# Performance work log

Hardware: AMD Instinct MI355X
Metric: run time of the kernel (lower is better)

The kernel has to match this reference:

```python
import jax, jax.numpy as jnp
import numpy as np

# Paged/ragged causal prefill attention (FlashInfer wrapper.run semantics),
# modeled as equal-length batched causal GQA attention.
B, S = 2, 2048          # batch, seq_len (T = B*S tokens, flattened)
H, HKV, D = 32, 8, 128  # query heads, kv heads, head dim
G = H // HKV            # GQA group size
SCALE = 0.08838834764831845  # 1/sqrt(D)


def setup_inputs() -> dict:
    key = jax.random.key(0)
    kq, kk, kv = jax.random.split(key, 3)
    q = jax.random.normal(kq, (B * S, H * D), dtype=jnp.float32)
    k = jax.random.normal(kk, (B * S, HKV * D), dtype=jnp.float32)
    v = jax.random.normal(kv, (B * S, HKV * D), dtype=jnp.float32)
    return {"q": q, "k": k, "v": v}


def reference(q, k, v):
    # q: [T, H*D] -> [B, S, HKV, G, D]; k, v: [T, HKV*D] -> [B, S, HKV, D]
    qh = q.reshape(B, S, HKV, G, D)
    kh = k.reshape(B, S, HKV, D)
    vh = v.reshape(B, S, HKV, D)
    # GQA attention scores: [B, HKV, G, Sq, Sk]
    scores = jnp.einsum('bqhgd,bkhd->bhgqk', qh, kh) * SCALE
    causal = jnp.tril(jnp.ones((S, S), dtype=bool))  # query attends to keys <= its position
    scores = jnp.where(causal, scores, jnp.finfo(scores.dtype).min)
    probs = jax.nn.softmax(scores, axis=-1)
    out = jnp.einsum('bhgqk,bkhd->bqhgd', probs, vh)
    # back to flattened token layout [T, H*D]
    return out.reshape(B * S, H * D)
```

## Files before the change

### kernel.cpp

```cpp
#include <hip/hip_runtime.h>


#define B_   2
#define S_   2048
#define H_   32
#define HKV_ 8
#define D_   128
#define SCALEF 0.08838834764831845f
#define COEF  (SCALEF * 1.44269504088896340736f)
#define DEFER_THR 8.0f

typedef float          f32x4 __attribute__((ext_vector_type(4)));
typedef __bf16         bf16x4 __attribute__((ext_vector_type(4)));
typedef __bf16         bf16x8 __attribute__((ext_vector_type(8)));
typedef unsigned short u16x8 __attribute__((ext_vector_type(8)));

#define MFMA16(a, b, c) __builtin_amdgcn_mfma_f32_16x16x32_bf16((a), (b), (c), 0, 0, 0)

#if defined(__has_builtin)
#if __has_builtin(__builtin_amdgcn_exp2f)
#define EXP2F(x) __builtin_amdgcn_exp2f(x)
#endif
#endif
#ifndef EXP2F
#define EXP2F(x) exp2f(x)
#endif

static __device__ __forceinline__ unsigned short f2bf(float f) {
  unsigned int u = __builtin_bit_cast(unsigned int, f);
  u = (u + 0x7fffu + ((u >> 16) & 1u)) >> 16;
  return (unsigned short)u;
}

static __device__ __forceinline__ void load_lds16(const void* g, void* l) {
  __builtin_amdgcn_global_load_lds(
      (const __attribute__((address_space(1))) void*)g,
      (__attribute__((address_space(3))) void*)l, 16, 0, 0);
}

static __device__ __forceinline__ float swz_x16(float v) {
  return __builtin_bit_cast(
      float, __builtin_amdgcn_ds_swizzle(__builtin_bit_cast(int, v), 0x401F));
}
static __device__ __forceinline__ float bperm_f(int byteaddr, float v) {
  return __builtin_bit_cast(
      float,
      __builtin_amdgcn_ds_bpermute(byteaddr, __builtin_bit_cast(int, v)));
}

__global__ __launch_bounds__(256) void prep_kernel(
    const float* __restrict__ k, const float* __restrict__ v,
    unsigned short* __restrict__ kbf, unsigned short* __restrict__ vt) {
  __shared__ float tile[32][65];
  const int tid = threadIdx.x;
  const int gid = (int)blockIdx.x;
  if (gid < 2048) {
    int t = gid * 256 + tid;
    int o = t * 8;
    int d = o & (D_ - 1);
    int s = (o >> 7) & (S_ - 1);
    int bh = o >> 18;
    int b = bh >> 3, hkv = bh & 7;
    const float* src = k + (size_t)(b * S_ + s) * (HKV_ * D_) + hkv * D_ + d;
    f32x4 x0 = *(const f32x4*)src;
    f32x4 x1 = *(const f32x4*)(src + 4);
    u16x8 w;
    w[0] = f2bf(x0[0]); w[1] = f2bf(x0[1]); w[2] = f2bf(x0[2]); w[3] = f2bf(x0[3]);
    w[4] = f2bf(x1[0]); w[5] = f2bf(x1[1]); w[6] = f2bf(x1[2]); w[7] = f2bf(x1[3]);
    *(u16x8*)(kbf + o) = w;
  } else {
    const int t = gid - 2048;
    const int s0 = (t & 31) * 64;
    const int d0 = ((t >> 5) & 3) * 32;
    const int bh = t >> 7;
    const float* src = v + (size_t)(bh >> 3) * S_ * (HKV_ * D_) + (bh & 7) * D_;
#pragma unroll
    for (int it = 0; it < 8; ++it) {
      int idx = it * 256 + tid;
      int sl = idx >> 5, dl = idx & 31;
      tile[dl][sl] = src[(size_t)(s0 + sl) * (HKV_ * D_) + d0 + dl];
    }
    __syncthreads();
    unsigned int* dst = (unsigned int*)vt;
#pragma unroll
    for (int it = 0; it < 4; ++it) {
      int idx = it * 256 + tid;
      int dl = idx >> 5, sp = idx & 31;
      unsigned int w = (unsigned int)f2bf(tile[dl][2 * sp]) |
                       ((unsigned int)f2bf(tile[dl][2 * sp + 1]) << 16);
      dst[(((size_t)bh * D_ + d0 + dl) * S_ + s0 + 2 * sp) >> 1] = w;
    }
  }
}

__global__ __launch_bounds__(256, 4) void attn_kernel(
    const float* __restrict__ qg, const unsigned short* __restrict__ kbfg,
    const unsigned short* __restrict__ vtg, float* __restrict__ outg) {
  __shared__ unsigned short KL[2][32 * 128];
  __shared__ unsigned short VL[2][128 * 32];

  const int tid = threadIdx.x;
  const int wave = tid >> 6, lane = tid & 63;
  const int l15 = lane & 15, quad = lane >> 4;
  const int a32 = ((lane ^ 32) << 2);
  const int rowa = quad << 4;

  const int id = (int)blockIdx.x + 16 * (int)blockIdx.y;
  const int xcd = id & 7, slot = id >> 3;
  const int bhkv = xcd * 2 + (slot >> 6);
  const int inner = slot & 63;
  const int g = inner >> 4;
  const int xb = inner & 15;
  const int b = bhkv >> 3, hkv = bhkv & 7;
  const int h = hkv * 4 + g;

  const unsigned short* kbf = kbfg + (size_t)(b * HKV_ + hkv) * S_ * D_;
  const unsigned short* vtb = vtg + (size_t)(b * HKV_ + hkv) * D_ * S_;

  const f32x4 zero4 = {0.f, 0.f, 0.f, 0.f};
  const float NEG_INF = -__builtin_huge_valf();

  auto stage = [&](int kt, int buf) {
#pragma unroll
    for (int j = 0; j < 2; ++j) {
      int si = wave * 128 + j * 64 + lane;
      int kr = si >> 4, pc = si & 15;
      int lc = pc ^ (kr & 15);
      int gs = ((kr & 15) >> 2) * 8 + ((kr >> 4) << 2) + (kr & 3);
      load_lds16(kbf + (size_t)(kt * 32 + gs) * D_ + lc * 8,
                 &KL[buf][(wave * 128 + j * 64) * 8]);
    }
#pragma unroll
    for (int j = 0; j < 2; ++j) {
      int si = wave * 128 + j * 64 + lane;
      int dr = si >> 2, pc = si & 3;
      int lc = pc ^ ((dr >> 1) & 3);
      load_lds16(vtb + (size_t)dr * S_ + kt * 32 + lc * 8,
                 &VL[buf][(wave * 128 + j * 64) * 8]);
    }
  };

  for (int ph = 0; ph < 2; ++ph) {
    const int qb = ph ? (31 - xb) : xb;
    const int qbase = qb * 64 + wave * 16;
    const int qgp = qbase + l15;

    bf16x8 qf[4];
#pragma unroll
    for (int ch = 0; ch < 4; ++ch) {
      const float* p = qg + (size_t)(b * S_ + qbase + l15) * (H_ * D_) +
                       h * D_ + ch * 32 + quad * 8;
      f32x4 x0 = *(const f32x4*)p;
      f32x4 x1 = *(const f32x4*)(p + 4);
      bf16x8 t;
      t[0] = (__bf16)(x0[0] * COEF); t[1] = (__bf16)(x0[1] * COEF);
      t[2] = (__bf16)(x0[2] * COEF); t[3] = (__bf16)(x0[3] * COEF);
      t[4] = (__bf16)(x1[0] * COEF); t[5] = (__bf16)(x1[1] * COEF);
      t[6] = (__bf16)(x1[2] * COEF); t[7] = (__bf16)(x1[3] * COEF);
      qf[ch] = t;
    }

    f32x4 acc[8];
#pragma unroll
    for (int dt = 0; dt < 8; ++dt) acc[dt] = zero4;
    float mrow = NEG_INF;
    float lsum = 0.f;

    const int nkt = qb * 2 + 2;

    stage(0, 0);
    __syncthreads();

#define KITER(KT, CUR)                                                        \
  do {                                                                        \
    const int kt_ = (KT);                                                     \
    if (kt_ + 1 < nkt) stage(kt_ + 1, (CUR) ^ 1);                             \
    if (kt_ * 32 <= qbase + 15) {                                             \
      f32x4 sc[2] = {zero4, zero4};                                           \
      __builtin_amdgcn_s_setprio(1);                                          \
      _Pragma("unroll") for (int h2 = 0; h2 < 2; ++h2) {                      \
        const int row = h2 * 16 + l15;                                        \
        _Pragma("unroll") for (int ch = 0; ch < 4; ++ch) {                    \
          const int pc = (ch * 4 + quad) ^ l15;               \
          u16x8 kf = *(const u16x8*)&KL[(CUR)][row * D_ + pc * 8];            \
          sc[h2] = MFMA16(__builtin_bit_cast(bf16x8, kf), qf[ch], sc[h2]);    \
        }                                                                     \
      }                                                                       \
      __builtin_amdgcn_s_setprio(0);                                          \
      const int kb0 = kt_ * 32;                                               \
                       \
      _Pragma("unroll") for (int h2 = 0; h2 < 2; ++h2) {                      \
        if (kb0 + 27 + h2 * 4 > qbase) {                                      \
          int kb2 = kb0 + quad * 8 + h2 * 4;                                  \
          _Pragma("unroll") for (int r = 0; r < 4; ++r) {                     \
            if (kb2 + r > qgp) sc[h2][r] = NEG_INF;                           \
          }                                                                   \
        }                                                                     \
      }                                                                       \
                      \
      float l8 = fmaxf(fmaxf(fmaxf(sc[0][0], sc[0][1]),                       \
                             fmaxf(sc[0][2], sc[0][3])),                      \
                       fmaxf(fmaxf(sc[1][0], sc[1][1]),                       \
                             fmaxf(sc[1][2], sc[1][3])));                     \
      if (!__all(l8 <= mrow + DEFER_THR)) {                                   \
        float t = fmaxf(l8, swz_x16(l8));             \
        t = fmaxf(t, bperm_f(a32, t));                                        \
        float mn = fmaxf(mrow, t);                                            \
        float al = EXP2F(mrow - mn);                                          \
        mrow = mn;                                                            \
        lsum *= al;                                                           \
        f32x4 av;       \
        _Pragma("unroll") for (int r = 0; r < 4; ++r)                         \
            av[r] = bperm_f(rowa + (r << 2), al);                             \
        _Pragma("unroll") for (int dt = 0; dt < 8; ++dt)                      \
            _Pragma("unroll") for (int r = 0; r < 4; ++r)                     \
                acc[dt][r] *= av[r];                                          \
      }                                                                       \
                         \
      _Pragma("unroll") for (int h2 = 0; h2 < 2; ++h2)                        \
          _Pragma("unroll") for (int r = 0; r < 4; ++r)                       \
              sc[h2][r] = EXP2F(sc[h2][r] - mrow);                            \
      lsum += ((sc[0][0] + sc[0][1]) + (sc[0][2] + sc[0][3])) +               \
              ((sc[1][0] + sc[1][1]) + (sc[1][2] + sc[1][3]));                \
             \
      bf16x8 pb;                                                              \
      pb[0] = (__bf16)sc[0][0]; pb[1] = (__bf16)sc[0][1];                     \
      pb[2] = (__bf16)sc[0][2]; pb[3] = (__bf16)sc[0][3];                     \
      pb[4] = (__bf16)sc[1][0]; pb[5] = (__bf16)sc[1][1];                     \
      pb[6] = (__bf16)sc[1][2]; pb[7] = (__bf16)sc[1][3];                     \
                       \
      {                                                                       \
        const int vsw = (quad ^ ((l15 >> 1) & 3)) * 8;                        \
        __builtin_amdgcn_s_setprio(1);                                        \
        _Pragma("unroll") for (int dt = 0; dt < 8; ++dt) {                    \
          u16x8 vf = *(const u16x8*)&VL[(CUR)][(dt * 16 + l15) * 32 + vsw];   \
          acc[dt] = MFMA16(pb, __builtin_bit_cast(bf16x8, vf), acc[dt]);      \
        }                                                                     \
        __builtin_amdgcn_s_setprio(0);                                        \
      }                                                                       \
    }                                                                         \
    __syncthreads();  \
  } while (0)

    for (int kt = 0; kt < nkt; kt += 2) {
      KITER(kt, 0);
      KITER(kt + 1, 1);
    }
#undef KITER

    float s = lsum;
    s += swz_x16(s);
    s += bperm_f(a32, s);
    float linv = 1.0f / s;
    f32x4 inv;
#pragma unroll
    for (int r = 0; r < 4; ++r) inv[r] = bperm_f(rowa + (r << 2), linv);
#pragma unroll
    for (int dt = 0; dt < 8; ++dt)
#pragma unroll
      for (int r = 0; r < 4; ++r)
        outg[(size_t)(b * S_ + qbase + quad * 4 + r) * (H_ * D_) +
             h * D_ + dt * 16 + l15] = acc[dt][r] * inv[r];
  }
}

extern "C" void kernel_launch(void* const* d_in, const int* in_sizes, int n_in,
                              void* d_out, int out_size, void* d_ws,
                              size_t ws_size, hipStream_t stream) {
  const float* q = (const float*)d_in[0];
  const float* k = (const float*)d_in[1];
  const float* v = (const float*)d_in[2];
  float* out = (float*)d_out;
  unsigned short* kws = (unsigned short*)d_ws;
  unsigned short* vtws = kws + (size_t)B_ * HKV_ * S_ * D_;

  prep_kernel<<<4096, 256, 0, stream>>>(k, v, kws, vtws);

  dim3 g2(16, B_ * H_);
  attn_kernel<<<g2, 256, 0, stream>>>(q, kws, vtws, out);
}
```

Baseline: 221.2 us.

## Software-pipeline QK^T of next tile with softmax and PV of previous tile

Restructures the KV loop so each iteration computes QK^T scores for the current tile while running softmax and PV on the previous tile's scores, which overlaps MFMA work with exp/reduction work. V moves to a triple-buffered LDS ring so the previous tile's V stays resident while the next one is being staged. This costs extra LDS and registers for the second score set, which may lower occupancy, and adds a tail step after the loop plus a barrier at the start of each phase.

After: 227.7 us. 1.03x slower.

```diff
diff --git a/kernel.cpp b/kernel.cpp
--- a/kernel.cpp
+++ b/kernel.cpp
@@ -97,7 +97,7 @@
     const float* __restrict__ qg, const unsigned short* __restrict__ kbfg,
     const unsigned short* __restrict__ vtg, float* __restrict__ outg) {
   __shared__ unsigned short KL[2][32 * 128];
-  __shared__ unsigned short VL[2][128 * 32];
+  __shared__ unsigned short VL[3][128 * 32];
 
   const int tid = threadIdx.x;
   const int wave = tid >> 6, lane = tid & 63;
@@ -120,7 +120,7 @@
   const f32x4 zero4 = {0.f, 0.f, 0.f, 0.f};
   const float NEG_INF = -__builtin_huge_valf();
 
-  auto stage = [&](int kt, int buf) {
+  auto stage = [&](int kt, int kbuf, int vbuf) {
 #pragma unroll
     for (int j = 0; j < 2; ++j) {
       int si = wave * 128 + j * 64 + lane;
@@ -128,7 +128,7 @@
       int lc = pc ^ (kr & 15);
       int gs = ((kr & 15) >> 2) * 8 + ((kr >> 4) << 2) + (kr & 3);
       load_lds16(kbf + (size_t)(kt * 32 + gs) * D_ + lc * 8,
-                 &KL[buf][(wave * 128 + j * 64) * 8]);
+                 &KL[kbuf][(wave * 128 + j * 64) * 8]);
     }
 #pragma unroll
     for (int j = 0; j < 2; ++j) {
@@ -136,7 +136,7 @@
       int dr = si >> 2, pc = si & 3;
       int lc = pc ^ ((dr >> 1) & 3);
       load_lds16(vtb + (size_t)dr * S_ + kt * 32 + lc * 8,
-                 &VL[buf][(wave * 128 + j * 64) * 8]);
+                 &VL[vbuf][(wave * 128 + j * 64) * 8]);
     }
   };
 
@@ -144,6 +144,9 @@
     const int qb = ph ? (31 - xb) : xb;
     const int qbase = qb * 64 + wave * 16;
     const int qgp = qbase + l15;
+
+    __syncthreads();
+    stage(0, 0, 0);
 
     bf16x8 qf[4];
 #pragma unroll
@@ -168,22 +171,68 @@
 
     const int nkt = qb * 2 + 2;
 
-    stage(0, 0);
+    f32x4 scA[2], scB[2];
+    int gprev = 0;
+    int vprev = 2, vcur = 0, vstage = 1;
+
     __syncthreads();
 
-#define KITER(KT, CUR)                                                        \
+#define SOFTPV(SC)                                                            \
+  do {                                                                        \
+    float l8 = fmaxf(fmaxf(fmaxf(SC[0][0], SC[0][1]),                         \
+                           fmaxf(SC[0][2], SC[0][3])),                        \
+                     fmaxf(fmaxf(SC[1][0], SC[1][1]),                         \
+                           fmaxf(SC[1][2], SC[1][3])));                       \
+    if (!__all(l8 <= mrow + DEFER_THR)) {                                     \
+      float t = fmaxf(l8, swz_x16(l8));               \
+      t = fmaxf(t, bperm_f(a32, t));                                          \
+      float mn = fmaxf(mrow, t);                                              \
+      float al = EXP2F(mrow - mn);                                            \
+      mrow = mn;                                                              \
+      lsum *= al;                                                             \
+      f32x4 av;         \
+      _Pragma("unroll") for (int r = 0; r < 4; ++r)                           \
+          av[r] = bperm_f(rowa + (r << 2), al);                               \
+      _Pragma("unroll") for (int dt = 0; dt < 8; ++dt)                        \
+          _Pragma("unroll") for (int r = 0; r < 4; ++r)                       \
+              acc[dt][r] *= av[r];                                            \
+    }                                                                         \
+    _Pragma("unroll") for (int h2 = 0; h2 < 2; ++h2)                          \
+        _Pragma("unroll") for (int r = 0; r < 4; ++r)                         \
+            SC[h2][r] = EXP2F(SC[h2][r] - mrow);                              \
+    lsum += ((SC[0][0] + SC[0][1]) + (SC[0][2] + SC[0][3])) +                 \
+            ((SC[1][0] + SC[1][1]) + (SC[1][2] + SC[1][3]));                  \
+    bf16x8 pb;               \
+    pb[0] = (__bf16)SC[0][0]; pb[1] = (__bf16)SC[0][1];                       \
+    pb[2] = (__bf16)SC[0][2]; pb[3] = (__bf16)SC[0][3];                       \
+    pb[4] = (__bf16)SC[1][0]; pb[5] = (__bf16)SC[1][1];                       \
+    pb[6] = (__bf16)SC[1][2]; pb[7] = (__bf16)SC[1][3];                       \
+    {                                                                         \
+      const unsigned short* vb_ = &VL[vprev][0];                              \
+      const int vsw = (quad ^ ((l15 >> 1) & 3)) * 8;        \
+      __builtin_amdgcn_s_setprio(1);                                          \
+      _Pragma("unroll") for (int dt = 0; dt < 8; ++dt) {                      \
+        u16x8 vf = *(const u16x8*)&vb_[(dt * 16 + l15) * 32 + vsw];           \
+        acc[dt] = MFMA16(pb, __builtin_bit_cast(bf16x8, vf), acc[dt]);        \
+      }                                                                       \
+      __builtin_amdgcn_s_setprio(0);                                          \
+    }                                                                         \
+  } while (0)
+
+#define PIPE(KT, PAR, SCN, SCO)                                               \
   do {                                                                        \
     const int kt_ = (KT);                                                     \
-    if (kt_ + 1 < nkt) stage(kt_ + 1, (CUR) ^ 1);                             \
-    if (kt_ * 32 <= qbase + 15) {                                             \
-      f32x4 sc[2] = {zero4, zero4};                                           \
+    if (kt_ + 1 < nkt) stage(kt_ + 1, (PAR) ^ 1, vstage);                     \
+    const int gcur = (kt_ * 32 <= qbase + 15) ? 1 : 0;                        \
+    if (gcur) {                                                               \
+      SCN[0] = zero4; SCN[1] = zero4;                                         \
       __builtin_amdgcn_s_setprio(1);                                          \
       _Pragma("unroll") for (int h2 = 0; h2 < 2; ++h2) {                      \
         const int row = h2 * 16 + l15;                                        \
         _Pragma("unroll") for (int ch = 0; ch < 4; ++ch) {                    \
           const int pc = (ch * 4 + quad) ^ l15;               \
-          u16x8 kf = *(const u16x8*)&KL[(CUR)][row * D_ + pc * 8];            \
-          sc[h2] = MFMA16(__builtin_bit_cast(bf16x8, kf), qf[ch], sc[h2]);    \
+          u16x8 kf = *(const u16x8*)&KL[(PAR)][row * D_ + pc * 8];            \
+          SCN[h2] = MFMA16(__builtin_bit_cast(bf16x8, kf), qf[ch], SCN[h2]);  \
         }                                                                     \
       }                                                                       \
       __builtin_amdgcn_s_setprio(0);                                          \
@@ -193,60 +242,24 @@
         if (kb0 + 27 + h2 * 4 > qbase) {                                      \
           int kb2 = kb0 + quad * 8 + h2 * 4;                                  \
           _Pragma("unroll") for (int r = 0; r < 4; ++r) {                     \
-            if (kb2 + r > qgp) sc[h2][r] = NEG_INF;                           \
+            if (kb2 + r > qgp) SCN[h2][r] = NEG_INF;                          \
           }                                                                   \
         }                                                                     \
       }                                                                       \
-                      \
-      float l8 = fmaxf(fmaxf(fmaxf(sc[0][0], sc[0][1]),                       \
-                             fmaxf(sc[0][2], sc[0][3])),                      \
-                       fmaxf(fmaxf(sc[1][0], sc[1][1]),                       \
-                             fmaxf(sc[1][2], sc[1][3])));                     \
-      if (!__all(l8 <= mrow + DEFER_THR)) {                                   \
-        float t = fmaxf(l8, swz_x16(l8));             \
-        t = fmaxf(t, bperm_f(a32, t));                                        \
-        float mn = fmaxf(mrow, t);                                            \
-        float al = EXP2F(mrow - mn);                                          \
-        mrow = mn;                                                            \
-        lsum *= al;                                                           \
-        f32x4 av;       \
-        _Pragma("unroll") for (int r = 0; r < 4; ++r)                         \
-            av[r] = bperm_f(rowa + (r << 2), al);                             \
-        _Pragma("unroll") for (int dt = 0; dt < 8; ++dt)                      \
-            _Pragma("unroll") for (int r = 0; r < 4; ++r)                     \
-                acc[dt][r] *= av[r];                                          \
-      }                                                                       \
-                         \
-      _Pragma("unroll") for (int h2 = 0; h2 < 2; ++h2)                        \
-          _Pragma("unroll") for (int r = 0; r < 4; ++r)                       \
-              sc[h2][r] = EXP2F(sc[h2][r] - mrow);                            \
-      lsum += ((sc[0][0] + sc[0][1]) + (sc[0][2] + sc[0][3])) +               \
-              ((sc[1][0] + sc[1][1]) + (sc[1][2] + sc[1][3]));                \
-             \
-      bf16x8 pb;                                                              \
-      pb[0] = (__bf16)sc[0][0]; pb[1] = (__bf16)sc[0][1];                     \
-      pb[2] = (__bf16)sc[0][2]; pb[3] = (__bf16)sc[0][3];                     \
-      pb[4] = (__bf16)sc[1][0]; pb[5] = (__bf16)sc[1][1];                     \
-      pb[6] = (__bf16)sc[1][2]; pb[7] = (__bf16)sc[1][3];                     \
-                       \
-      {                                                                       \
-        const int vsw = (quad ^ ((l15 >> 1) & 3)) * 8;                        \
-        __builtin_amdgcn_s_setprio(1);                                        \
-        _Pragma("unroll") for (int dt = 0; dt < 8; ++dt) {                    \
-          u16x8 vf = *(const u16x8*)&VL[(CUR)][(dt * 16 + l15) * 32 + vsw];   \
-          acc[dt] = MFMA16(pb, __builtin_bit_cast(bf16x8, vf), acc[dt]);      \
-        }                                                                     \
-        __builtin_amdgcn_s_setprio(0);                                        \
-      }                                                                       \
     }                                                                         \
-    __syncthreads();  \
+    if (gprev) SOFTPV(SCO);                                                   \
+    gprev = gcur;                                                             \
+    vprev = vcur; vcur = vstage; vstage = (vstage == 2) ? 0 : vstage + 1;     \
+    __syncthreads();       \
   } while (0)
 
     for (int kt = 0; kt < nkt; kt += 2) {
-      KITER(kt, 0);
-      KITER(kt + 1, 1);
-    }
-#undef KITER
+      PIPE(kt, 0, scA, scB);
+      PIPE(kt + 1, 1, scB, scA);
+    }
+    if (gprev) SOFTPV(scB);
+#undef PIPE
+#undef SOFTPV
 
     float s = lsum;
     s += swz_x16(s);
```
